# Optimization experiments

Hardware: AMD Instinct MI355X
Metric: run time of the kernel (lower is better)

## Reference

```python
import jax, jax.numpy as jnp
import numpy as np

N_NODES = 50000
N_EDGES = 800000
DIM = 256
HEADS = 8
DIM_OUT = 32  # per-head; dim_inner = HEADS*DIM_OUT = 256


def setup_inputs() -> dict:
    key = jax.random.key(0)
    ks = jax.random.split(key, 9)
    s = 1.0 / np.sqrt(DIM)
    inner = HEADS * DIM_OUT
    return {
        "x": jax.random.normal(ks[0], (N_NODES, DIM), dtype=jnp.float32),
        "Wq": jax.random.uniform(ks[1], (DIM, inner), jnp.float32, -s, s),
        "bq": jax.random.uniform(ks[2], (inner,), jnp.float32, -s, s),
        "Wk": jax.random.uniform(ks[3], (DIM, inner), jnp.float32, -s, s),
        "bk": jax.random.uniform(ks[4], (inner,), jnp.float32, -s, s),
        "Wv": jax.random.uniform(ks[5], (DIM, inner), jnp.float32, -s, s),
        "bv": jax.random.uniform(ks[6], (inner,), jnp.float32, -s, s),
        "src": jax.random.randint(ks[7], (N_EDGES,), 0, N_NODES),
        "dst": jax.random.randint(ks[8], (N_EDGES,), 0, N_NODES),
    }


def reference(x, Wq, bq, Wk, bk, Wv, bv, src, dst):
    n = x.shape[0]
    q = (x @ Wq + bq).reshape(n, HEADS, DIM_OUT)
    k = (x @ Wk + bk).reshape(n, HEADS, DIM_OUT)
    v = (x @ Wv + bv).reshape(n, HEADS, DIM_OUT)
    # edge-wise u_dot_v: dot of src query with dst key, per head -> [E, H]
    scores = jnp.einsum('ehd,ehd->eh', q[src], k[dst]) / jnp.sqrt(
        jnp.asarray(DIM_OUT, dtype=x.dtype))
    # segment softmax over incoming edges of each destination node
    m = jax.ops.segment_max(scores, dst, num_segments=n)  # [N, H]
    m = jnp.where(jnp.isfinite(m), m, 0.0)
    e = jnp.exp(scores - m[dst])
    z = jax.ops.segment_sum(e, dst, num_segments=n)  # [N, H]
    p = e / jnp.maximum(z[dst], 1e-16)  # [E, H]
    # u_mul_e_sum: sum over incoming edges of src values weighted by attn
    out = jax.ops.segment_sum(v[src] * p[:, :, None], dst, num_segments=n)
    return out.reshape(n, HEADS * DIM_OUT)  # concat=True
```

## Files before the change

kernel.cpp:

```cpp
#include <hip/hip_runtime.h>
#include <math.h>

#define N_NODES 50000
#define N_EDGES 800000
#define DIM 256
#define HEADS 8
#define DIM_OUT 32
#define INNER 256
#define M_PAD 50048

typedef __attribute__((ext_vector_type(8))) short bf16x8;
typedef __attribute__((ext_vector_type(4))) float f32x4;
typedef __attribute__((ext_vector_type(2))) float f32x2;

__device__ __forceinline__ unsigned short f2bf(float f) {
    unsigned u = __float_as_uint(f);
    unsigned r = (u + 0x7FFFu + ((u >> 16) & 1u)) >> 16;
    return (unsigned short)r;
}

__device__ __forceinline__ f32x2 up2(unsigned u) {
    f32x2 r;
    r.x = __uint_as_float(u << 16);
    r.y = __uint_as_float(u & 0xFFFF0000u);
    return r;
}
__device__ __forceinline__ void up2x4(uint4 r, f32x2* o) {
    o[0] = up2(r.x); o[1] = up2(r.y); o[2] = up2(r.z); o[3] = up2(r.w);
}

__device__ __forceinline__ void gll16(const void* g, void* l) {
    __builtin_amdgcn_global_load_lds(
        (const __attribute__((address_space(1))) unsigned*)(uintptr_t)g,
        (__attribute__((address_space(3))) unsigned*)(unsigned)(uintptr_t)l,
        16, 0, 0);
}

#define NB_CONVX 6256
#define NB_CONVW 768
#define NB_HIST  3125
__global__ __launch_bounds__(256) void prep(
    const float* __restrict__ x,
    const float* __restrict__ Wq, const float* __restrict__ Wk,
    const float* __restrict__ Wv,
    const int* __restrict__ dst,
    unsigned short* __restrict__ xbf, unsigned short* __restrict__ Wt,
    int* __restrict__ deg)
{
    int b = blockIdx.x;
    if (b < NB_CONVX) {
        size_t i8 = ((size_t)b * 256 + threadIdx.x) * 8;
        unsigned short h[8];
        if (i8 < (size_t)N_NODES * 256) {
            float4 a = *(const float4*)(x + i8);
            float4 c = *(const float4*)(x + i8 + 4);
            h[0]=f2bf(a.x); h[1]=f2bf(a.y); h[2]=f2bf(a.z); h[3]=f2bf(a.w);
            h[4]=f2bf(c.x); h[5]=f2bf(c.y); h[6]=f2bf(c.z); h[7]=f2bf(c.w);
        } else {
            #pragma unroll
            for (int j = 0; j < 8; j++) h[j] = 0;
        }
        uint4 o;
        o.x = (unsigned)h[0] | ((unsigned)h[1] << 16);
        o.y = (unsigned)h[2] | ((unsigned)h[3] << 16);
        o.z = (unsigned)h[4] | ((unsigned)h[5] << 16);
        o.w = (unsigned)h[6] | ((unsigned)h[7] << 16);
        *(uint4*)(xbf + i8) = o;
    } else if (b < NB_CONVX + NB_CONVW) {
        int idx = (b - NB_CONVX) * 256 + threadIdx.x;
        int z = idx >> 16, r = idx & 65535;
        int k = r >> 8, n = r & 255;
        const float* W = (z == 0) ? Wq : (z == 1) ? Wk : Wv;
        Wt[(size_t)z * 65536 + n * 256 + k] = f2bf(W[k * 256 + n]);
    } else {
        int e = (b - NB_CONVX - NB_CONVW) * 256 + threadIdx.x;
        if (e < N_EDGES) atomicAdd(deg + dst[e], 1);
    }
}

__global__ __launch_bounds__(256) void gemm_qkv(
    const unsigned short* __restrict__ xbf,
    const unsigned short* __restrict__ Wt,
    const float* __restrict__ bq, const float* __restrict__ bk,
    const float* __restrict__ bv,
    unsigned short* __restrict__ q, unsigned short* __restrict__ k,
    unsigned short* __restrict__ v)
{
    const int t = threadIdx.x;
    const int row0 = blockIdx.x * 128;
    const int col0 = blockIdx.y * 128;
    const int z = blockIdx.z;
    const unsigned short* Wz = Wt + (size_t)z * 65536;
    const float* bias = (z == 0) ? bq : (z == 1) ? bk : bv;
    unsigned short* C = (z == 0) ? q : (z == 1) ? k : v;

    __shared__ __align__(16) short As[128 * 32];
    __shared__ __align__(16) short Bs[128 * 32];

    const int wave = t >> 6;
    const int lane = t & 63;
    const int wm = (wave & 1) * 64;
    const int wn = (wave >> 1) * 64;
    const int lr = lane & 15;
    const int lg = lane >> 4;
    const int srow = lane >> 2;
    const int sch  = lane & 3;

    f32x4 acc[4][4] = {};

    for (int k0 = 0; k0 < 256; k0 += 32) {
        #pragma unroll
        for (int c = 0; c < 2; c++) {
            int seg = wave * 2 + c;
            gll16(xbf + (size_t)(row0 + seg * 16 + srow) * 256 + k0 + sch * 8,
                  As + seg * 512);
        }
        #pragma unroll
        for (int c = 0; c < 2; c++) {
            int seg = wave * 2 + c;
            gll16(Wz + (size_t)(col0 + seg * 16 + srow) * 256 + k0 + sch * 8,
                  Bs + seg * 512);
        }
        __syncthreads();

        bf16x8 af[4], bfr[4];
        #pragma unroll
        for (int mi = 0; mi < 4; mi++)
            af[mi] = *(const bf16x8*)&As[(wm + mi * 16 + lr) * 32 + lg * 8];
        #pragma unroll
        for (int ni = 0; ni < 4; ni++)
            bfr[ni] = *(const bf16x8*)&Bs[(wn + ni * 16 + lr) * 32 + lg * 8];
        #pragma unroll
        for (int mi = 0; mi < 4; mi++)
            #pragma unroll
            for (int ni = 0; ni < 4; ni++)
                acc[mi][ni] = __builtin_amdgcn_mfma_f32_16x16x32_bf16(
                    af[mi], bfr[ni], acc[mi][ni], 0, 0, 0);
        __syncthreads();
    }

    #pragma unroll
    for (int mi = 0; mi < 4; mi++) {
        #pragma unroll
        for (int ni = 0; ni < 4; ni++) {
            int gcol = col0 + wn + ni * 16 + lr;
            float bb = bias[gcol];
            #pragma unroll
            for (int r = 0; r < 4; r++) {
                int grow = row0 + wm + mi * 16 + lg * 4 + r;
                if (grow < N_NODES)
                    C[(size_t)grow * 256 + gcol] = f2bf(acc[mi][ni][r] + bb);
            }
        }
    }
}

__global__ __launch_bounds__(1024) void scan_deg(
    const int* __restrict__ deg, int* __restrict__ rowptr)
{
    __shared__ int wsum[16];
    __shared__ int wpre[16];
    int t = threadIdx.x;
    int wid = t >> 6, ln = t & 63;
    int carry = 0;
    for (int base = 0; base < N_NODES; base += 4096) {
        int i4 = base + t * 4;
        int4 dv = {0, 0, 0, 0};
        if (i4 < N_NODES) dv = *(const int4*)(deg + i4);
        int sum = dv.x + dv.y + dv.z + dv.w;
        int inc = sum;
        #pragma unroll
        for (int off = 1; off < 64; off <<= 1) {
            int u = __shfl_up(inc, off);
            if (ln >= off) inc += u;
        }
        if (ln == 63) wsum[wid] = inc;
        __syncthreads();
        if (wid == 0 && ln < 16) {
            int s = wsum[ln];
            int p = s;
            #pragma unroll
            for (int off = 1; off < 16; off <<= 1) {
                int u = __shfl_up(p, off);
                if (ln >= off) p += u;
            }
            wpre[ln] = p - s;
        }
        __syncthreads();
        if (i4 < N_NODES) {
            int r = carry + wpre[wid] + (inc - sum);
            r += dv.x; rowptr[i4 + 1] = r;
            r += dv.y; rowptr[i4 + 2] = r;
            r += dv.z; rowptr[i4 + 3] = r;
            r += dv.w; rowptr[i4 + 4] = r;
        }
        carry += wpre[15] + wsum[15];
        __syncthreads();
    }
    if (t == 0) rowptr[0] = 0;
}

__global__ __launch_bounds__(256) void csr_scatter(
    const int* __restrict__ src, const int* __restrict__ dst,
    const int* __restrict__ rowptr,
    int* __restrict__ deg, int* __restrict__ edge_src)
{
    int e = blockIdx.x * 256 + threadIdx.x;
    if (e >= N_EDGES) return;
    int d = dst[e];
    int old = atomicSub(deg + d, 1);
    edge_src[rowptr[d] + old - 1] = src[e];
}

__global__ __launch_bounds__(256) void node_attn(
    const unsigned short* __restrict__ qbf,
    const unsigned short* __restrict__ kbf,
    const unsigned short* __restrict__ vbf,
    const int* __restrict__ rowptr, const int* __restrict__ edge_src,
    float* __restrict__ out)
{
    int node = blockIdx.x * 4 + (threadIdx.x >> 6);
    int lane = threadIdx.x & 63;
    if (node >= N_NODES) return;
    const int half = lane >> 5;
    const int l = lane & 31;

    f32x2 kf2[4];
    up2x4(*(const uint4*)(kbf + (size_t)node * 256 + l * 8), kf2);

    int beg = rowptr[node], end = rowptr[node + 1];

    float m = -INFINITY, zsum = 0.0f;
    f32x2 af2[4] = {};

    int i0 = beg + half;
    bool va0 = i0 < end;
    bool va1 = (i0 + 2) < end;
    bool va2 = (i0 + 4) < end;
    int s0 = va0 ? edge_src[i0] : 0;
    int s1 = va1 ? edge_src[i0 + 2] : 0;
    int s2 = va2 ? edge_src[i0 + 4] : 0;
    uint4 q0 = {}, v0 = {}, q1 = {}, v1 = {};
    if (va0) {
        q0 = *(const uint4*)(qbf + (size_t)s0 * 256 + l * 8);
        v0 = *(const uint4*)(vbf + (size_t)s0 * 256 + l * 8);
    }
    if (va1) {
        q1 = *(const uint4*)(qbf + (size_t)s1 * 256 + l * 8);
        v1 = *(const uint4*)(vbf + (size_t)s1 * 256 + l * 8);
    }
    int ii = i0 + 6;

    while (va0) {
        uint4 q2 = {}, v2 = {};
        if (va2) {
            q2 = *(const uint4*)(qbf + (size_t)s2 * 256 + l * 8);
            v2 = *(const uint4*)(vbf + (size_t)s2 * 256 + l * 8);
        }
        bool va3 = ii < end;
        int s3 = va3 ? edge_src[ii] : 0;
        ii += 2;

        f32x2 qf2[4], vf2[4];
        up2x4(q0, qf2);
        up2x4(v0, vf2);
        f32x2 d2 = qf2[0] * kf2[0];
        d2 += qf2[1] * kf2[1];
        d2 += qf2[2] * kf2[2];
        d2 += qf2[3] * kf2[3];
        float t = d2.x + d2.y;
        t += __shfl_xor(t, 1);
        t += __shfl_xor(t, 2);
        float sc = t * 0.17677669529663687f;
        float mn = fmaxf(m, sc);
        float alpha = __expf(m - mn);
        float w = __expf(sc - mn);
        zsum = zsum * alpha + w;
        f32x2 a2 = {alpha, alpha};
        f32x2 w2 = {w, w};
        #pragma unroll
        for (int j = 0; j < 4; j++) af2[j] = af2[j] * a2 + vf2[j] * w2;
        m = mn;

        q0 = q1; v0 = v1; q1 = q2; v1 = v2;
        s2 = s3;
        va0 = va1; va1 = va2; va2 = va3;
    }

    float mo = __shfl_xor(m, 32);
    float mt = fmaxf(m, mo);
    float scale = (m == -INFINITY) ? 0.0f : __expf(m - mt);
    zsum *= scale;
    zsum += __shfl_xor(zsum, 32);
    #pragma unroll
    for (int j = 0; j < 4; j++) {
        af2[j].x = af2[j].x * scale;
        af2[j].y = af2[j].y * scale;
        af2[j].x += __shfl_xor(af2[j].x, 32);
        af2[j].y += __shfl_xor(af2[j].y, 32);
    }

    float inv = 1.0f / fmaxf(zsum, 1e-16f);
    if (half == 0) {
        float4 o0 = {af2[0].x * inv, af2[0].y * inv, af2[1].x * inv, af2[1].y * inv};
        float4 o1 = {af2[2].x * inv, af2[2].y * inv, af2[3].x * inv, af2[3].y * inv};
        float* op = out + (size_t)node * 256 + l * 8;
        *(float4*)op = o0;
        *(float4*)(op + 4) = o1;
    }
}

extern "C" void kernel_launch(void* const* d_in, const int* in_sizes, int n_in,
                              void* d_out, int out_size, void* d_ws, size_t ws_size,
                              hipStream_t stream) {
    const float* x  = (const float*)d_in[0];
    const float* Wq = (const float*)d_in[1];
    const float* bq = (const float*)d_in[2];
    const float* Wk = (const float*)d_in[3];
    const float* bk = (const float*)d_in[4];
    const float* Wv = (const float*)d_in[5];
    const float* bv = (const float*)d_in[6];
    const int* src  = (const int*)d_in[7];
    const int* dst  = (const int*)d_in[8];
    float* out = (float*)d_out;

    unsigned short* qbf = (unsigned short*)d_ws;
    unsigned short* kbf = qbf + (size_t)N_NODES * INNER;
    unsigned short* vbf = kbf + (size_t)N_NODES * INNER;
    unsigned short* xbf = vbf + (size_t)N_NODES * INNER;
    unsigned short* Wt  = xbf + (size_t)M_PAD * INNER;
    int* deg      = (int*)(Wt + 3 * 65536);
    int* rowptr   = deg + N_NODES;
    int* edge_src = rowptr + (N_NODES + 1);

    hipMemsetAsync(deg, 0, (size_t)N_NODES * sizeof(int), stream);

    prep<<<NB_CONVX + NB_CONVW + NB_HIST, 256, 0, stream>>>(
        x, Wq, Wk, Wv, dst, xbf, Wt, deg);

    dim3 gg(M_PAD / 128, 2, 3);
    gemm_qkv<<<gg, 256, 0, stream>>>(xbf, Wt, bq, bk, bv, qbf, kbf, vbf);

    scan_deg<<<1, 1024, 0, stream>>>(deg, rowptr);
    csr_scatter<<<(N_EDGES + 255) / 256, 256, 0, stream>>>(
        src, dst, rowptr, deg, edge_src);

    node_attn<<<(N_NODES + 3) / 4, 256, 0, stream>>>(
        qbf, kbf, vbf, rowptr, edge_src, out);
}
```

Before: 373.5 us.

## Remap GEMM blocks per XCD and rotate-pipeline the node attention gather loop

The QKV GEMM now launches a flat 1D grid and remaps block IDs so that consecutive logical tiles, which share the same x rows across the six column/weight tiles, run on the same XCD for better L2 reuse. The attention kernel now writes zeros early for nodes with no incoming edges. Its gather loop is replaced by a branch-free, 3-way rotated register pipeline with clamped indices, a wave-uniform trip count, masking of out-of-range edges, and exp2 with a pre-folded log2e scale. This is meant to hide gather latency and remove per-edge divergent branches, at the cost of some wasted masked iterations and redundant loads of the clamped last edge.

```diff
diff --git a/kernel.cpp b/kernel.cpp
--- a/kernel.cpp
+++ b/kernel.cpp
@@ -78,6 +78,7 @@
     }
 }
 
+#define GEMM_NWG 2346
 __global__ __launch_bounds__(256) void gemm_qkv(
     const unsigned short* __restrict__ xbf,
     const unsigned short* __restrict__ Wt,
@@ -86,10 +87,17 @@
     unsigned short* __restrict__ q, unsigned short* __restrict__ k,
     unsigned short* __restrict__ v)
 {
+    int hw = blockIdx.x;
+    int xcd = hw & 7, pos = hw >> 3;
+    const int q8 = GEMM_NWG >> 3, r8 = GEMM_NWG & 7;
+    int lid = (xcd < r8 ? xcd * (q8 + 1) : r8 * (q8 + 1) + (xcd - r8) * q8) + pos;
+    int xx = lid / 6;
+    int yz = lid - xx * 6;
+    const int row0 = xx * 128;
+    const int col0 = (yz & 1) * 128;
+    const int z = yz >> 1;
+
     const int t = threadIdx.x;
-    const int row0 = blockIdx.x * 128;
-    const int col0 = blockIdx.y * 128;
-    const int z = blockIdx.z;
     const unsigned short* Wz = Wt + (size_t)z * 65536;
     const float* bias = (z == 0) ? bq : (z == 1) ? bk : bv;
     unsigned short* C = (z == 0) ? q : (z == 1) ? k : v;
@@ -225,71 +233,90 @@
     const int half = lane >> 5;
     const int l = lane & 31;
 
+    int beg = rowptr[node], end = rowptr[node + 1];
+    int deg = end - beg;
+
+    float* op = out + (size_t)node * 256 + l * 8;
+    if (deg <= 0) {
+        if (half == 0) {
+            float4 z4 = {0.f, 0.f, 0.f, 0.f};
+            *(float4*)op = z4;
+            *(float4*)(op + 4) = z4;
+        }
+        return;
+    }
+
     f32x2 kf2[4];
     up2x4(*(const uint4*)(kbf + (size_t)node * 256 + l * 8), kf2);
 
-    int beg = rowptr[node], end = rowptr[node + 1];
-
-    float m = -INFINITY, zsum = 0.0f;
+    const unsigned short* qrow = qbf + l * 8;
+    const unsigned short* vrow = vbf + l * 8;
+
+    const float SC = 0.17677669529663687f * 1.4426950408889634f;
+
+    int U = (deg + 1) >> 1;
+    U = ((U + 2) / 3) * 3;
+    U = __builtin_amdgcn_readfirstlane(U);
+
+    const int i0 = beg + half;
+    const int last = end - 1;
+
+    int tmp0 = edge_src[min(i0,     last)];
+    int tmp1 = edge_src[min(i0 + 2, last)];
+    int idC  = edge_src[min(i0 + 4, last)];
+    int idA  = edge_src[min(i0 + 6, last)];
+    int idB  = 0;
+    uint4 qA = *(const uint4*)(qrow + (size_t)tmp0 * 256);
+    uint4 vA = *(const uint4*)(vrow + (size_t)tmp0 * 256);
+    uint4 qB = *(const uint4*)(qrow + (size_t)tmp1 * 256);
+    uint4 vB = *(const uint4*)(vrow + (size_t)tmp1 * 256);
+    uint4 qC, vC;
+
+    float m = -1e30f, zsum = 0.0f;
     f32x2 af2[4] = {};
 
-    int i0 = beg + half;
-    bool va0 = i0 < end;
-    bool va1 = (i0 + 2) < end;
-    bool va2 = (i0 + 4) < end;
-    int s0 = va0 ? edge_src[i0] : 0;
-    int s1 = va1 ? edge_src[i0 + 2] : 0;
-    int s2 = va2 ? edge_src[i0 + 4] : 0;
-    uint4 q0 = {}, v0 = {}, q1 = {}, v1 = {};
-    if (va0) {
-        q0 = *(const uint4*)(qbf + (size_t)s0 * 256 + l * 8);
-        v0 = *(const uint4*)(vbf + (size_t)s0 * 256 + l * 8);
-    }
-    if (va1) {
-        q1 = *(const uint4*)(qbf + (size_t)s1 * 256 + l * 8);
-        v1 = *(const uint4*)(vbf + (size_t)s1 * 256 + l * 8);
-    }
-    int ii = i0 + 6;
-
-    while (va0) {
-        uint4 q2 = {}, v2 = {};
-        if (va2) {
-            q2 = *(const uint4*)(qbf + (size_t)s2 * 256 + l * 8);
-            v2 = *(const uint4*)(vbf + (size_t)s2 * 256 + l * 8);
-        }
-        bool va3 = ii < end;
-        int s3 = va3 ? edge_src[ii] : 0;
-        ii += 2;
-
-        f32x2 qf2[4], vf2[4];
-        up2x4(q0, qf2);
-        up2x4(v0, vf2);
-        f32x2 d2 = qf2[0] * kf2[0];
-        d2 += qf2[1] * kf2[1];
-        d2 += qf2[2] * kf2[2];
-        d2 += qf2[3] * kf2[3];
-        float t = d2.x + d2.y;
-        t += __shfl_xor(t, 1);
-        t += __shfl_xor(t, 2);
-        float sc = t * 0.17677669529663687f;
-        float mn = fmaxf(m, sc);
-        float alpha = __expf(m - mn);
-        float w = __expf(sc - mn);
-        zsum = zsum * alpha + w;
-        f32x2 a2 = {alpha, alpha};
-        f32x2 w2 = {w, w};
-        #pragma unroll
-        for (int j = 0; j < 4; j++) af2[j] = af2[j] * a2 + vf2[j] * w2;
-        m = mn;
-
-        q0 = q1; v0 = v1; q1 = q2; v1 = v2;
-        s2 = s3;
-        va0 = va1; va1 = va2; va2 = va3;
-    }
+#define BODY(QW, VW, QL, VL, IDL, IDF, P)                                    \
+    do {                                                                     \
+        size_t off_ = (size_t)(IDL) * 256;                                   \
+        QL = *(const uint4*)(qrow + off_);                                   \
+        VL = *(const uint4*)(vrow + off_);                                   \
+        int vi_ = i0 + 2 * t + 2 * (P);                                      \
+        IDF = edge_src[min(vi_ + 8, last)];                                  \
+        f32x2 qf_[4], vf_[4];                                                \
+        up2x4(QW, qf_);                                                      \
+        up2x4(VW, vf_);                                                      \
+        f32x2 d_ = qf_[0] * kf2[0];                                          \
+        d_ += qf_[1] * kf2[1];                                               \
+        d_ += qf_[2] * kf2[2];                                               \
+        d_ += qf_[3] * kf2[3];                                               \
+        float s_ = d_.x + d_.y;                                              \
+        s_ += __shfl_xor(s_, 1);                                             \
+        s_ += __shfl_xor(s_, 2);                                             \
+        bool ok_ = vi_ < end;                                                \
+        float sc_ = ok_ ? s_ * SC : -1e30f;                                  \
+        float mn_ = fmaxf(m, sc_);                                           \
+        float w_ = exp2f(sc_ - mn_);                                         \
+        w_ = ok_ ? w_ : 0.0f;                                                \
+        float al_ = exp2f(m - mn_);                                          \
+        zsum = zsum * al_ + w_;                                              \
+        f32x2 a2_ = {al_, al_}, w2_ = {w_, w_};                              \
+        af2[0] = af2[0] * a2_ + vf_[0] * w2_;                                \
+        af2[1] = af2[1] * a2_ + vf_[1] * w2_;                                \
+        af2[2] = af2[2] * a2_ + vf_[2] * w2_;                                \
+        af2[3] = af2[3] * a2_ + vf_[3] * w2_;                                \
+        m = mn_;                                                             \
+    } while (0)
+
+    for (int t = 0; t < U; t += 3) {
+        BODY(qA, vA, qC, vC, idC, idB, 0);
+        BODY(qB, vB, qA, vA, idA, idC, 1);
+        BODY(qC, vC, qB, vB, idB, idA, 2);
+    }
+#undef BODY
 
     float mo = __shfl_xor(m, 32);
     float mt = fmaxf(m, mo);
-    float scale = (m == -INFINITY) ? 0.0f : __expf(m - mt);
+    float scale = exp2f(m - mt);
     zsum *= scale;
     zsum += __shfl_xor(zsum, 32);
     #pragma unroll
@@ -304,7 +331,6 @@
     if (half == 0) {
         float4 o0 = {af2[0].x * inv, af2[0].y * inv, af2[1].x * inv, af2[1].y * inv};
         float4 o1 = {af2[2].x * inv, af2[2].y * inv, af2[3].x * inv, af2[3].y * inv};
-        float* op = out + (size_t)node * 256 + l * 8;
         *(float4*)op = o0;
         *(float4*)(op + 4) = o1;
     }
@@ -338,8 +364,7 @@
     prep<<<NB_CONVX + NB_CONVW + NB_HIST, 256, 0, stream>>>(
         x, Wq, Wk, Wv, dst, xbf, Wt, deg);
 
-    dim3 gg(M_PAD / 128, 2, 3);
-    gemm_qkv<<<gg, 256, 0, stream>>>(xbf, Wt, bq, bk, bv, qbf, kbf, vbf);
+    gemm_qkv<<<GEMM_NWG, 256, 0, stream>>>(xbf, Wt, bq, bk, bv, qbf, kbf, vbf);
 
     scan_deg<<<1, 1024, 0, stream>>>(deg, rowptr);
     csr_scatter<<<(N_EDGES + 255) / 256, 256, 0, stream>>>(
```

After: 366.6 us. About the same (-1.8%).
